# Optimization experiments

Hardware: AMD Instinct MI355X
Metric: run time of the kernel (lower is better)

Reference implementation:

```python
import jax, jax.numpy as jnp
import numpy as np

SMOOTH = 1e-3
N_BASES = 256


def _bases():
    # bases[i, k] = k-th bit (LSB-first) of i, matching f'{i:08b}'[::-1]
    i = np.arange(N_BASES)[:, None]
    k = np.arange(8)[None, :]
    return jnp.asarray(((i >> k) & 1).astype(np.float32))  # [256, 8]


def _unfold(x):
    # x: [B, 2, Y, X] -> [B, 8, (Y+1)*(X+1)], matching F.unfold(kernel=(2,2), padding=1)
    B, C, Y, X = x.shape
    p = jnp.pad(x, ((0, 0), (0, 0), (1, 1), (1, 1)))
    cols = [p[:, c, ky:ky + Y + 1, kx:kx + X + 1]
            for c in range(2) for ky in range(2) for kx in range(2)]
    return jnp.stack(cols, axis=1).reshape(B, 8, (Y + 1) * (X + 1))


def _pair(pred_s, labels, raw, area, bases):
    # pred_s/labels/raw: [B, 2, Y, X]
    up = _unfold(pred_s)                       # [B, 8, L] sigmoid probs
    ul = _unfold(labels)                       # [B, 8, L] float 0/1
    ur = _unfold(raw)                          # [B, 8, L] logits
    uli = ul.astype(jnp.int32)
    B, _, L = up.shape

    # 8-bit neighbour code per point
    label_byte = sum(uli[:, k, :] << k for k in range(8))  # [B, L] int32

    # pred weight of the basis matching each point's label code (gather form of the masked loop)
    sel = bases[label_byte]                    # [B, L, 8]
    w_lab = 1.0 - jnp.linalg.norm(up.transpose(0, 2, 1) - sel, axis=-1) / 16.0  # [B, L]

    # sequential 256-way byte update, faithful to the original python loop
    up_sg = jax.lax.stop_gradient(up)
    d2 = ((up_sg ** 2).sum(1)[:, None, :]
          - 2.0 * jnp.einsum('bkl,nk->bnl', up_sg, bases)
          + (bases ** 2).sum(1)[None, :, None])              # [B, 256, L]
    w_all = 1.0 - jnp.sqrt(jnp.maximum(d2, 0.0)) / 16.0      # [B, 256, L]

    def body(i, byte):
        w = w_all[:, i, :]
        return jnp.where(w > byte.astype(w.dtype), jnp.full_like(byte, 0) + i, byte)

    pred_byte = jax.lax.fori_loop(0, N_BASES, body, jnp.zeros((B, L), jnp.int32))

    pred_areas = area[pred_byte]               # [B, L]
    label_areas = area[label_byte]             # [B, L]
    num = 2.0 * (w_lab * label_areas).sum(1)   # [B]
    denom = label_areas.sum(1) + pred_areas.sum(1)

    # per-batch BCE-with-logits on points whose label cube is empty or full
    mask = ((label_byte == 0) | (label_byte == 255)).astype(up.dtype)  # [B, L]
    x, y = ur, ul
    bce = jnp.maximum(x, 0.0) - x * y + jnp.log1p(jnp.exp(-jnp.abs(x)))  # [B, 8, L]
    vol = (bce * mask[:, None, :]).sum((1, 2)) / (8.0 * mask.sum(1))     # [B]
    return num, denom, vol


def _forward(pred, labels, area):
    pred_s = jax.nn.sigmoid(pred)
    bases = _bases()
    # overlapping z-pairs: [B, Z-1, 2, Y, X] -> vmap over pair axis
    ps = jnp.stack((pred_s[:, :-1], pred_s[:, 1:]), axis=2)
    ls = jnp.stack((labels[:, :-1], labels[:, 1:]), axis=2)
    rs = jnp.stack((pred[:, :-1], pred[:, 1:]), axis=2)
    num, denom, vol = jax.vmap(lambda a, b, c: _pair(a, b, c, area, bases),
                               in_axes=1)(ps, ls, rs)
    num, denom, vol = num.sum(0), denom.sum(0), vol.sum(0)  # [B]
    dice = 1.0 - (num + SMOOTH) / (denom + SMOOTH)
    return dice.mean() + vol.mean()


def setup_inputs() -> dict:
    key = jax.random.key(0)
    k1, k2, k3 = jax.random.split(key, 3)
    pred = jax.random.normal(k1, (2, 12, 192, 192), dtype=jnp.float32)
    labels = jax.random.bernoulli(k2, 0.5, (2, 12, 192, 192)).astype(jnp.float32)
    area = jax.random.uniform(k3, (256,), dtype=jnp.float32) * 2.0
    return {"pred": pred, "labels": labels, "area": area}


def reference(pred, labels, area):
    return _forward(pred, labels, area)
```

## Files before the change

### kernel.cpp

```cpp
#include <hip/hip_runtime.h>
#include <math.h>

#define NYX 192
#define NNODE 193
#define L_NODES (NNODE*NNODE)
#define NPAIR 11
#define NB 2
#define NCH 12
#define NGRP (NPAIR*NB)
#define NBLK 49
#define LN2f 0.69314718055994530942f


__global__ __launch_bounds__(256) void sdice_node(const float* __restrict__ pred,
                                                  const float* __restrict__ labels,
                                                  const float* __restrict__ area,
                                                  float4* __restrict__ partials)
{
    const int pair = blockIdx.z;
    const int b    = blockIdx.y;
    const int lane = threadIdx.x & 63;
    const int wrow = threadIdx.x >> 6;
    const int j    = blockIdx.x * 4 + wrow;
    const int t    = lane;

    __shared__ float areas[256];
    __shared__ float sred[4][4];
    areas[threadIdx.x] = area[threadIdx.x];
    __syncthreads();

    float num = 0.f, den = 0.f, bces = 0.f, cnt = 0.f;
    const bool act = (j < NNODE) && (t < 48);

    if (act) {
        float sig6[4][6], bcv6[4][6];
        unsigned w5[4];

        const int  y0 = (j >= 1) ? (j - 1) : 0;
        const int  y1 = (j <= NYX - 1) ? j : (NYX - 1);
        const bool m0 = (j >= 1);
        const bool m1 = (j <= NYX - 1);
        const int  xo = t * 4;

        #pragma unroll
        for (int c = 0; c < 2; ++c) {
            const size_t base = (size_t)(b * NCH + pair + c) * (NYX * NYX);
            #pragma unroll
            for (int r = 0; r < 2; ++r) {
                const int  cr = c * 2 + r;
                const int  yy = r ? y1 : y0;
                const bool mm = r ? m1 : m0;
                const float4 p4 = *reinterpret_cast<const float4*>(pred   + base + (size_t)yy * NYX + xo);
                const float4 l4 = *reinterpret_cast<const float4*>(labels + base + (size_t)yy * NYX + xo);
                const float pe[4] = {p4.x, p4.y, p4.z, p4.w};
                const float le[4] = {l4.x, l4.y, l4.z, l4.w};
                unsigned bits = 0;
                #pragma unroll
                for (int e = 0; e < 4; ++e) {
                    const float pv = mm ? pe[e] : 0.f;
                    const float lv = mm ? le[e] : 0.f;
                    bits |= ((unsigned)lv) << e;
                    const float s = __builtin_amdgcn_rcpf(1.f + __expf(-pv));
                    sig6[cr][e + 1] = mm ? s : 0.f;
                    bcv6[cr][e + 1] = fmaxf(pv, 0.f) - pv * lv + __logf(1.f + __expf(-fabsf(pv)));
                }
                w5[cr] = bits << 1;
                sig6[cr][5] = 0.f;
                bcv6[cr][5] = LN2f;
            }
        }

        #pragma unroll
        for (int cr = 0; cr < 4; ++cr) {
            const float    sw = __shfl_up(sig6[cr][4], 1);
            const float    bw = __shfl_up(bcv6[cr][4], 1);
            const unsigned ww = (unsigned)__shfl_up((int)w5[cr], 1);
            sig6[cr][0] = (t == 0) ? 0.f  : sw;
            bcv6[cr][0] = (t == 0) ? LN2f : bw;
            w5[cr]     |= (t == 0) ? 0u   : ((ww >> 4) & 1u);
        }

        #pragma unroll
        for (int i = 0; i < 5; ++i) {
            if (i < 4 || t == 47) {
                unsigned byte = 0;
                float d2 = 0.f, bsum = 0.f;
                #pragma unroll
                for (int cr = 0; cr < 4; ++cr) {
                    const unsigned bp = (w5[cr] >> i) & 1u;
                    const unsigned bc = (w5[cr] >> (i + 1)) & 1u;
                    byte |= (bp << (2 * cr)) | (bc << (2 * cr + 1));
                    const float dp = sig6[cr][i]     - (float)bp;
                    const float dc = sig6[cr][i + 1] - (float)bc;
                    d2   += dp * dp + dc * dc;
                    bsum += bcv6[cr][i] + bcv6[cr][i + 1];
                }
                const float w  = 1.f - sqrtf(d2) * (1.f / 16.f);
                const float la = areas[byte];
                num += w * la;
                den += la;
                const bool msk = (byte == 0u) || (byte == 255u);
                cnt  += msk ? 1.f : 0.f;
                bces += msk ? bsum : 0.f;
            }
        }
    }

    #pragma unroll
    for (int off = 32; off > 0; off >>= 1) {
        num  += __shfl_down(num, off);
        den  += __shfl_down(den, off);
        bces += __shfl_down(bces, off);
        cnt  += __shfl_down(cnt, off);
    }
    if (lane == 0) { sred[wrow][0] = num; sred[wrow][1] = den; sred[wrow][2] = bces; sred[wrow][3] = cnt; }
    __syncthreads();
    if (threadIdx.x == 0) {
        float n = 0, d = 0, bc = 0, ct = 0;
        #pragma unroll
        for (int w = 0; w < 4; ++w) { n += sred[w][0]; d += sred[w][1]; bc += sred[w][2]; ct += sred[w][3]; }
        partials[(size_t)(pair * NB + b) * NBLK + blockIdx.x] = make_float4(n, d, bc, ct);
    }
}

__global__ __launch_bounds__(256) void sdice_final(const float4* __restrict__ partials,
                                                   const float* __restrict__ area,
                                                   float* __restrict__ out)
{
    __shared__ float gs[NGRP][4];
    const int wid  = threadIdx.x >> 6;
    const int lane = threadIdx.x & 63;

    for (int g = wid; g < NGRP; g += 4) {
        float n = 0.f, d = 0.f, bc = 0.f, ct = 0.f;
        for (int i = lane; i < NBLK; i += 64) {
            const float4 v = partials[(size_t)g * NBLK + i];
            n += v.x; d += v.y; bc += v.z; ct += v.w;
        }
        #pragma unroll
        for (int off = 32; off > 0; off >>= 1) {
            n  += __shfl_down(n, off);
            d  += __shfl_down(d, off);
            bc += __shfl_down(bc, off);
            ct += __shfl_down(ct, off);
        }
        if (lane == 0) { gs[g][0] = n; gs[g][1] = d; gs[g][2] = bc; gs[g][3] = ct; }
    }
    __syncthreads();
    if (threadIdx.x == 0) {
        const float a1 = area[1];
        float dice_sum = 0.f, vol_sum = 0.f;
        for (int b = 0; b < NB; ++b) {
            float numb = 0.f, denb = 0.f, volb = 0.f;
            for (int p = 0; p < NPAIR; ++p) {
                const int g = p * NB + b;
                numb += 2.0f * gs[g][0];
                denb += gs[g][1] + (float)L_NODES * a1;
                volb += gs[g][2] / (8.0f * gs[g][3]);
            }
            dice_sum += 1.0f - (numb + 0.001f) / (denb + 0.001f);
            vol_sum  += volb;
        }
        out[0] = dice_sum / (float)NB + vol_sum / (float)NB;
    }
}

extern "C" void kernel_launch(void* const* d_in, const int* in_sizes, int n_in,
                              void* d_out, int out_size, void* d_ws, size_t ws_size,
                              hipStream_t stream) {
    const float* pred   = (const float*)d_in[0];
    const float* labels = (const float*)d_in[1];
    const float* area   = (const float*)d_in[2];
    float* out = (float*)d_out;
    float4* part = (float4*)d_ws;

    dim3 grid(NBLK, NB, NPAIR);
    sdice_node<<<grid, dim3(256), 0, stream>>>(pred, labels, area, part);
    sdice_final<<<1, 256, 0, stream>>>(part, area, out);
}
```

Before: 19.40 us.

## Fuse final reduction into node kernel via atomics and last-block ticket

Removes the separate finalize kernel launch. Each block atomically adds its four partial sums into per-group accumulators and takes a ticket, and the last block to finish computes the final loss. A hipMemsetAsync zeroes the accumulators and the ticket before each launch. This trades one kernel launch for a memset plus global atomics, and float atomics make the summation order nondeterministic.

```diff
diff --git a/kernel.cpp b/kernel.cpp
--- a/kernel.cpp
+++ b/kernel.cpp
@@ -9,13 +9,17 @@
 #define NCH 12
 #define NGRP (NPAIR*NB)
 #define NBLK 49
+#define TOTAL_BLOCKS (NBLK*NB*NPAIR)
 #define LN2f 0.69314718055994530942f
 
+#define ACC_STRIDE 16
 
-__global__ __launch_bounds__(256) void sdice_node(const float* __restrict__ pred,
-                                                  const float* __restrict__ labels,
-                                                  const float* __restrict__ area,
-                                                  float4* __restrict__ partials)
+__global__ __launch_bounds__(256) void sdice_fused(const float* __restrict__ pred,
+                                                   const float* __restrict__ labels,
+                                                   const float* __restrict__ area,
+                                                   float* __restrict__ acc,
+                                                   unsigned* __restrict__ ticket,
+                                                   float* __restrict__ out)
 {
     const int pair = blockIdx.z;
     const int b    = blockIdx.y;
@@ -26,6 +30,8 @@
 
     __shared__ float areas[256];
     __shared__ float sred[4][4];
+    __shared__ int   isLast;
+    __shared__ float gs[NGRP][4];
     areas[threadIdx.x] = area[threadIdx.x];
     __syncthreads();
 
@@ -115,53 +121,46 @@
     }
     if (lane == 0) { sred[wrow][0] = num; sred[wrow][1] = den; sred[wrow][2] = bces; sred[wrow][3] = cnt; }
     __syncthreads();
+
     if (threadIdx.x == 0) {
         float n = 0, d = 0, bc = 0, ct = 0;
         #pragma unroll
         for (int w = 0; w < 4; ++w) { n += sred[w][0]; d += sred[w][1]; bc += sred[w][2]; ct += sred[w][3]; }
-        partials[(size_t)(pair * NB + b) * NBLK + blockIdx.x] = make_float4(n, d, bc, ct);
-    }
-}
-
-__global__ __launch_bounds__(256) void sdice_final(const float4* __restrict__ partials,
-                                                   const float* __restrict__ area,
-                                                   float* __restrict__ out)
-{
-    __shared__ float gs[NGRP][4];
-    const int wid  = threadIdx.x >> 6;
-    const int lane = threadIdx.x & 63;
-
-    for (int g = wid; g < NGRP; g += 4) {
-        float n = 0.f, d = 0.f, bc = 0.f, ct = 0.f;
-        for (int i = lane; i < NBLK; i += 64) {
-            const float4 v = partials[(size_t)g * NBLK + i];
-            n += v.x; d += v.y; bc += v.z; ct += v.w;
-        }
-        #pragma unroll
-        for (int off = 32; off > 0; off >>= 1) {
-            n  += __shfl_down(n, off);
-            d  += __shfl_down(d, off);
-            bc += __shfl_down(bc, off);
-            ct += __shfl_down(ct, off);
-        }
-        if (lane == 0) { gs[g][0] = n; gs[g][1] = d; gs[g][2] = bc; gs[g][3] = ct; }
+        float* g = acc + (size_t)(pair * NB + b) * ACC_STRIDE;
+        atomicAdd(g + 0, n);
+        atomicAdd(g + 1, d);
+        atomicAdd(g + 2, bc);
+        atomicAdd(g + 3, ct);
+        __threadfence();
+        const unsigned tk = atomicAdd(ticket, 1u);
+        isLast = (tk == TOTAL_BLOCKS - 1);
     }
     __syncthreads();
-    if (threadIdx.x == 0) {
-        const float a1 = area[1];
-        float dice_sum = 0.f, vol_sum = 0.f;
-        for (int b = 0; b < NB; ++b) {
-            float numb = 0.f, denb = 0.f, volb = 0.f;
-            for (int p = 0; p < NPAIR; ++p) {
-                const int g = p * NB + b;
-                numb += 2.0f * gs[g][0];
-                denb += gs[g][1] + (float)L_NODES * a1;
-                volb += gs[g][2] / (8.0f * gs[g][3]);
+
+    if (isLast) {
+        __threadfence();
+        if (threadIdx.x < NGRP * 4) {
+            const int g = threadIdx.x >> 2;
+            const int v = threadIdx.x & 3;
+            gs[g][v] = atomicAdd(acc + (size_t)g * ACC_STRIDE + v, 0.0f);
+        }
+        __syncthreads();
+        if (threadIdx.x == 0) {
+            const float a1 = areas[1];
+            float dice_sum = 0.f, vol_sum = 0.f;
+            for (int bb = 0; bb < NB; ++bb) {
+                float numb = 0.f, denb = 0.f, volb = 0.f;
+                for (int p = 0; p < NPAIR; ++p) {
+                    const int g = p * NB + bb;
+                    numb += 2.0f * gs[g][0];
+                    denb += gs[g][1] + (float)L_NODES * a1;
+                    volb += gs[g][2] / (8.0f * gs[g][3]);
+                }
+                dice_sum += 1.0f - (numb + 0.001f) / (denb + 0.001f);
+                vol_sum  += volb;
             }
-            dice_sum += 1.0f - (numb + 0.001f) / (denb + 0.001f);
-            vol_sum  += volb;
+            out[0] = dice_sum / (float)NB + vol_sum / (float)NB;
         }
-        out[0] = dice_sum / (float)NB + vol_sum / (float)NB;
     }
 }
 
@@ -172,9 +171,13 @@
     const float* labels = (const float*)d_in[1];
     const float* area   = (const float*)d_in[2];
     float* out = (float*)d_out;
-    float4* part = (float4*)d_ws;
+    char*  ws  = (char*)d_ws;
+
+    float*    acc    = (float*)ws;
+    unsigned* ticket = (unsigned*)(ws + NGRP * ACC_STRIDE * sizeof(float));
+
+    hipMemsetAsync(ws, 0, NGRP * ACC_STRIDE * sizeof(float) + sizeof(unsigned), stream);
 
     dim3 grid(NBLK, NB, NPAIR);
-    sdice_node<<<grid, dim3(256), 0, stream>>>(pred, labels, area, part);
-    sdice_final<<<1, 256, 0, stream>>>(part, area, out);
+    sdice_fused<<<grid, dim3(256), 0, stream>>>(pred, labels, area, acc, ticket, out);
 }
```

Result: slower. 36.21 us (+86.6%).

## Process multiple z-pairs per block, reusing channel loads and sigmoid/BCE terms

Applied to the files above, without the earlier changes.

Each block now walks a chunk of 4-5 consecutive channels and keeps the previous channel's sigmoid, BCE and label bits in registers. Adjacent z-pairs therefore no longer reload and recompute the shared channel. The grid shrinks from 11 pair slices to 3 z-chunks, which cuts global reads and transcendental work roughly in half. The cost is fewer blocks (294 versus 1078), a serial loop per thread, a 10-value reduction per block, and a reworked final kernel that handles per-pair volume terms.

```diff
diff --git a/kernel.cpp b/kernel.cpp
--- a/kernel.cpp
+++ b/kernel.cpp
@@ -7,49 +7,55 @@
 #define NPAIR 11
 #define NB 2
 #define NCH 12
-#define NGRP (NPAIR*NB)
+#define NZ 3
+#define NGRP (NZ*NB)
 #define NBLK 49
+#define RECF 12
 #define LN2f 0.69314718055994530942f
 
 
 __global__ __launch_bounds__(256) void sdice_node(const float* __restrict__ pred,
                                                   const float* __restrict__ labels,
                                                   const float* __restrict__ area,
-                                                  float4* __restrict__ partials)
+                                                  float* __restrict__ partials)
 {
-    const int pair = blockIdx.z;
+    const int z    = blockIdx.z;
     const int b    = blockIdx.y;
     const int lane = threadIdx.x & 63;
     const int wrow = threadIdx.x >> 6;
     const int j    = blockIdx.x * 4 + wrow;
     const int t    = lane;
+    const int np   = (z == 2) ? 3 : 4;
+    const int nch  = np + 1;
+    const int c0   = z * 4;
 
     __shared__ float areas[256];
-    __shared__ float sred[4][4];
+    __shared__ float sred[4][10];
     areas[threadIdx.x] = area[threadIdx.x];
     __syncthreads();
 
-    float num = 0.f, den = 0.f, bces = 0.f, cnt = 0.f;
+    float numA = 0.f, denA = 0.f;
+    float bceA[4] = {0.f, 0.f, 0.f, 0.f};
+    float cntA[4] = {0.f, 0.f, 0.f, 0.f};
+
     const bool act = (j < NNODE) && (t < 48);
 
     if (act) {
-        float sig6[4][6], bcv6[4][6];
-        unsigned w5[4];
-
         const int  y0 = (j >= 1) ? (j - 1) : 0;
         const int  y1 = (j <= NYX - 1) ? j : (NYX - 1);
-        const bool m0 = (j >= 1);
-        const bool m1 = (j <= NYX - 1);
         const int  xo = t * 4;
 
-        #pragma unroll
-        for (int c = 0; c < 2; ++c) {
-            const size_t base = (size_t)(b * NCH + pair + c) * (NYX * NYX);
+        float    sigP[2][6], bcvP[2][6], sigC[2][6], bcvC[2][6];
+        unsigned w5P[2], w5C[2];
+
+        for (int cc = 0; cc < nch; ++cc) {
+            const int ch = c0 + cc;
+            const size_t base = (size_t)(b * NCH + ch) * (NYX * NYX);
+
             #pragma unroll
             for (int r = 0; r < 2; ++r) {
-                const int  cr = c * 2 + r;
                 const int  yy = r ? y1 : y0;
-                const bool mm = r ? m1 : m0;
+                const bool mm = r ? (j <= NYX - 1) : (j >= 1);
                 const float4 p4 = *reinterpret_cast<const float4*>(pred   + base + (size_t)yy * NYX + xo);
                 const float4 l4 = *reinterpret_cast<const float4*>(labels + base + (size_t)yy * NYX + xo);
                 const float pe[4] = {p4.x, p4.y, p4.z, p4.w};
@@ -61,103 +67,135 @@
                     const float lv = mm ? le[e] : 0.f;
                     bits |= ((unsigned)lv) << e;
                     const float s = __builtin_amdgcn_rcpf(1.f + __expf(-pv));
-                    sig6[cr][e + 1] = mm ? s : 0.f;
-                    bcv6[cr][e + 1] = fmaxf(pv, 0.f) - pv * lv + __logf(1.f + __expf(-fabsf(pv)));
+                    sigC[r][e + 1] = mm ? s : 0.f;
+                    bcvC[r][e + 1] = fmaxf(pv, 0.f) - pv * lv + __logf(1.f + __expf(-fabsf(pv)));
                 }
-                w5[cr] = bits << 1;
-                sig6[cr][5] = 0.f;
-                bcv6[cr][5] = LN2f;
+                w5C[r] = bits << 1;
+                sigC[r][5] = 0.f;
+                bcvC[r][5] = LN2f;
+
+                const float    sw = __shfl_up(sigC[r][4], 1);
+                const float    bw = __shfl_up(bcvC[r][4], 1);
+                const unsigned ww = (unsigned)__shfl_up((int)w5C[r], 1);
+                sigC[r][0] = (t == 0) ? 0.f  : sw;
+                bcvC[r][0] = (t == 0) ? LN2f : bw;
+                w5C[r]    |= (t == 0) ? 0u   : ((ww >> 4) & 1u);
+            }
+
+            if (cc > 0) {
+                const int pp = cc - 1;
+                float pnum = 0.f, pden = 0.f, pbce = 0.f, pcnt = 0.f;
+                #pragma unroll
+                for (int i = 0; i < 5; ++i) {
+                    if (i < 4 || t == 47) {
+                        const unsigned b0 = (w5P[0] >> i) & 1u, b1 = (w5P[0] >> (i + 1)) & 1u;
+                        const unsigned b2 = (w5P[1] >> i) & 1u, b3 = (w5P[1] >> (i + 1)) & 1u;
+                        const unsigned b4 = (w5C[0] >> i) & 1u, b5 = (w5C[0] >> (i + 1)) & 1u;
+                        const unsigned b6 = (w5C[1] >> i) & 1u, b7 = (w5C[1] >> (i + 1)) & 1u;
+                        const unsigned byte = b0 | (b1 << 1) | (b2 << 2) | (b3 << 3)
+                                            | (b4 << 4) | (b5 << 5) | (b6 << 6) | (b7 << 7);
+                        float d2 = 0.f;
+                        {
+                            const float e0 = sigP[0][i]     - (float)b0;
+                            const float e1 = sigP[0][i + 1] - (float)b1;
+                            const float e2 = sigP[1][i]     - (float)b2;
+                            const float e3 = sigP[1][i + 1] - (float)b3;
+                            const float e4 = sigC[0][i]     - (float)b4;
+                            const float e5 = sigC[0][i + 1] - (float)b5;
+                            const float e6 = sigC[1][i]     - (float)b6;
+                            const float e7 = sigC[1][i + 1] - (float)b7;
+                            d2 = ((e0*e0 + e1*e1) + (e2*e2 + e3*e3)) + ((e4*e4 + e5*e5) + (e6*e6 + e7*e7));
+                        }
+                        const float w  = 1.f - sqrtf(d2) * (1.f / 16.f);
+                        const float la = areas[byte];
+                        pnum += w * la;
+                        pden += la;
+                        const bool msk = (byte == 0u) || (byte == 255u);
+                        if (msk) {
+                            pcnt += 1.f;
+                            pbce += ((bcvP[0][i] + bcvP[0][i+1]) + (bcvP[1][i] + bcvP[1][i+1]))
+                                  + ((bcvC[0][i] + bcvC[0][i+1]) + (bcvC[1][i] + bcvC[1][i+1]));
+                        }
+                    }
+                }
+                numA += pnum; denA += pden;
+                bceA[pp] += pbce; cntA[pp] += pcnt;
+            }
+
+            #pragma unroll
+            for (int r = 0; r < 2; ++r) {
+                w5P[r] = w5C[r];
+                #pragma unroll
+                for (int q = 0; q < 6; ++q) { sigP[r][q] = sigC[r][q]; bcvP[r][q] = bcvC[r][q]; }
             }
         }
-
-        #pragma unroll
-        for (int cr = 0; cr < 4; ++cr) {
-            const float    sw = __shfl_up(sig6[cr][4], 1);
-            const float    bw = __shfl_up(bcv6[cr][4], 1);
-            const unsigned ww = (unsigned)__shfl_up((int)w5[cr], 1);
-            sig6[cr][0] = (t == 0) ? 0.f  : sw;
-            bcv6[cr][0] = (t == 0) ? LN2f : bw;
-            w5[cr]     |= (t == 0) ? 0u   : ((ww >> 4) & 1u);
-        }
-
-        #pragma unroll
-        for (int i = 0; i < 5; ++i) {
-            if (i < 4 || t == 47) {
-                unsigned byte = 0;
-                float d2 = 0.f, bsum = 0.f;
-                #pragma unroll
-                for (int cr = 0; cr < 4; ++cr) {
-                    const unsigned bp = (w5[cr] >> i) & 1u;
-                    const unsigned bc = (w5[cr] >> (i + 1)) & 1u;
-                    byte |= (bp << (2 * cr)) | (bc << (2 * cr + 1));
-                    const float dp = sig6[cr][i]     - (float)bp;
-                    const float dc = sig6[cr][i + 1] - (float)bc;
-                    d2   += dp * dp + dc * dc;
-                    bsum += bcv6[cr][i] + bcv6[cr][i + 1];
-                }
-                const float w  = 1.f - sqrtf(d2) * (1.f / 16.f);
-                const float la = areas[byte];
-                num += w * la;
-                den += la;
-                const bool msk = (byte == 0u) || (byte == 255u);
-                cnt  += msk ? 1.f : 0.f;
-                bces += msk ? bsum : 0.f;
-            }
-        }
-    }
-
+    }
+
+
+    float v[10] = {numA, denA, bceA[0], bceA[1], bceA[2], bceA[3], cntA[0], cntA[1], cntA[2], cntA[3]};
     #pragma unroll
     for (int off = 32; off > 0; off >>= 1) {
-        num  += __shfl_down(num, off);
-        den  += __shfl_down(den, off);
-        bces += __shfl_down(bces, off);
-        cnt  += __shfl_down(cnt, off);
-    }
-    if (lane == 0) { sred[wrow][0] = num; sred[wrow][1] = den; sred[wrow][2] = bces; sred[wrow][3] = cnt; }
+        #pragma unroll
+        for (int q = 0; q < 10; ++q) v[q] += __shfl_down(v[q], off);
+    }
+    if (lane == 0) {
+        #pragma unroll
+        for (int q = 0; q < 10; ++q) sred[wrow][q] = v[q];
+    }
     __syncthreads();
     if (threadIdx.x == 0) {
-        float n = 0, d = 0, bc = 0, ct = 0;
-        #pragma unroll
-        for (int w = 0; w < 4; ++w) { n += sred[w][0]; d += sred[w][1]; bc += sred[w][2]; ct += sred[w][3]; }
-        partials[(size_t)(pair * NB + b) * NBLK + blockIdx.x] = make_float4(n, d, bc, ct);
+        float s[10];
+        #pragma unroll
+        for (int q = 0; q < 10; ++q)
+            s[q] = ((sred[0][q] + sred[1][q]) + (sred[2][q] + sred[3][q]));
+        float* rec = partials + (size_t)((z * NB + b) * NBLK + blockIdx.x) * RECF;
+        #pragma unroll
+        for (int q = 0; q < 10; ++q) rec[q] = s[q];
+        rec[10] = 0.f; rec[11] = 0.f;
     }
 }
 
-__global__ __launch_bounds__(256) void sdice_final(const float4* __restrict__ partials,
+__global__ __launch_bounds__(384) void sdice_final(const float* __restrict__ partials,
                                                    const float* __restrict__ area,
                                                    float* __restrict__ out)
 {
-    __shared__ float gs[NGRP][4];
-    const int wid  = threadIdx.x >> 6;
+    __shared__ float gs[NGRP][10];
+    const int g    = threadIdx.x >> 6;
     const int lane = threadIdx.x & 63;
 
-    for (int g = wid; g < NGRP; g += 4) {
-        float n = 0.f, d = 0.f, bc = 0.f, ct = 0.f;
-        for (int i = lane; i < NBLK; i += 64) {
-            const float4 v = partials[(size_t)g * NBLK + i];
-            n += v.x; d += v.y; bc += v.z; ct += v.w;
-        }
-        #pragma unroll
-        for (int off = 32; off > 0; off >>= 1) {
-            n  += __shfl_down(n, off);
-            d  += __shfl_down(d, off);
-            bc += __shfl_down(bc, off);
-            ct += __shfl_down(ct, off);
-        }
-        if (lane == 0) { gs[g][0] = n; gs[g][1] = d; gs[g][2] = bc; gs[g][3] = ct; }
+    float v[10];
+    #pragma unroll
+    for (int q = 0; q < 10; ++q) v[q] = 0.f;
+    if (lane < NBLK) {
+        const float* rec = partials + (size_t)(g * NBLK + lane) * RECF;
+        #pragma unroll
+        for (int q = 0; q < 10; ++q) v[q] = rec[q];
+    }
+    #pragma unroll
+    for (int off = 32; off > 0; off >>= 1) {
+        #pragma unroll
+        for (int q = 0; q < 10; ++q) v[q] += __shfl_down(v[q], off);
+    }
+    if (lane == 0) {
+        #pragma unroll
+        for (int q = 0; q < 10; ++q) gs[g][q] = v[q];
     }
     __syncthreads();
+
     if (threadIdx.x == 0) {
         const float a1 = area[1];
         float dice_sum = 0.f, vol_sum = 0.f;
         for (int b = 0; b < NB; ++b) {
             float numb = 0.f, denb = 0.f, volb = 0.f;
-            for (int p = 0; p < NPAIR; ++p) {
-                const int g = p * NB + b;
-                numb += 2.0f * gs[g][0];
-                denb += gs[g][1] + (float)L_NODES * a1;
-                volb += gs[g][2] / (8.0f * gs[g][3]);
-            }
+            for (int z = 0; z < NZ; ++z) {
+                const int g2 = z * NB + b;
+                const int np = (z == 2) ? 3 : 4;
+                numb += 2.0f * gs[g2][0];
+                denb += gs[g2][1];
+                for (int pp = 0; pp < np; ++pp)
+                    volb += gs[g2][2 + pp] / (8.0f * gs[g2][6 + pp]);
+            }
+            denb += (float)NPAIR * (float)L_NODES * a1;
             dice_sum += 1.0f - (numb + 0.001f) / (denb + 0.001f);
             vol_sum  += volb;
         }
@@ -171,10 +209,10 @@
     const float* pred   = (const float*)d_in[0];
     const float* labels = (const float*)d_in[1];
     const float* area   = (const float*)d_in[2];
-    float* out = (float*)d_out;
-    float4* part = (float4*)d_ws;
-
-    dim3 grid(NBLK, NB, NPAIR);
+    float* out  = (float*)d_out;
+    float* part = (float*)d_ws;
+
+    dim3 grid(NBLK, NB, NZ);
     sdice_node<<<grid, dim3(256), 0, stream>>>(pred, labels, area, part);
-    sdice_final<<<1, 256, 0, stream>>>(part, area, out);
+    sdice_final<<<1, 384, 0, stream>>>(part, area, out);
 }
```

New measurement: 19.23 us. About the same (-0.9%).
